# Kernel tuning notes

Measured on AMD Instinct MI355X. Metric: run time of the kernel, lower is better.

The kernel has to match this reference:

```python
import jax, jax.numpy as jnp
import numpy as np

B, N, D, H, HID = 8, 512, 512, 8, 2048


def setup_inputs() -> dict:
    key = jax.random.key(0)
    ks = jax.random.split(key, 8)
    s = 0.02
    p = lambda i, shape: jax.random.normal(ks[i], shape, jnp.float32) * s
    return dict(
        x=jax.random.normal(ks[0], (B, N, D), jnp.float32),
        Wq=p(1, (D, D)), bq=jnp.zeros((D,), jnp.float32),
        Wk=p(2, (D, D)), bk=jnp.zeros((D,), jnp.float32),
        Wv=p(3, (D, D)), bv=jnp.zeros((D,), jnp.float32),
        Wsig=p(4, (H, D)), bsig=jnp.zeros((H,), jnp.float32),
        ln1_g=jnp.ones((D,), jnp.float32), ln1_b=jnp.zeros((D,), jnp.float32),
        W1=p(5, (HID, D)), b1=jnp.zeros((HID,), jnp.float32),
        W2=p(6, (D, HID)), b2=jnp.zeros((D,), jnp.float32),
        ln2_g=jnp.ones((D,), jnp.float32), ln2_b=jnp.zeros((D,), jnp.float32),
    )


def _ln(z, g, b, eps=1e-5):
    m = jnp.mean(z, axis=-1, keepdims=True)
    v = jnp.var(z, axis=-1, keepdims=True)
    return (z - m) * jax.lax.rsqrt(v + eps) * g + b


def reference(x, Wq, bq, Wk, bk, Wv, bv, Wsig, bsig,
              ln1_g, ln1_b, W1, b1, W2, b2, ln2_g, ln2_b):
    Bb, Nn, Dd = x.shape
    Hh = bsig.shape[0]
    dh = Dd // Hh
    # --- AnomalyAttention: series attention S, Gaussian prior P, Z = S @ V ---
    Q = (x @ Wq.T + bq).reshape(Bb, Nn, Hh, dh)
    K = (x @ Wk.T + bk).reshape(Bb, Nn, Hh, dh)
    V = (x @ Wv.T + bv).reshape(Bb, Nn, Hh, dh)
    scores = jnp.einsum('bnhd,bmhd->bhnm', Q, K) / jnp.sqrt(jnp.float32(dh))
    S = jax.nn.softmax(scores, axis=-1)                       # [B,H,N,N]
    # learned positive scale sigma per (batch, position, head)
    sigma = jax.nn.softplus(x @ Wsig.T + bsig) + 1e-5         # [B,N,H]
    idx = jnp.arange(Nn, dtype=jnp.float32)
    dist2 = (idx[:, None] - idx[None, :]) ** 2                # [N,N]
    sig = jnp.transpose(sigma, (0, 2, 1))[..., None]          # [B,H,N,1]
    gauss = jnp.exp(-dist2 / (2.0 * sig * sig)) / (jnp.sqrt(2.0 * jnp.pi) * sig)
    P = gauss / jnp.sum(gauss, axis=-1, keepdims=True)        # row-normalized prior
    Zh = jnp.einsum('bhnm,bmhd->bnhd', S, V).reshape(Bb, Nn, Dd)
    # --- residual + LayerNorm + MLP(relu) + residual + LayerNorm ---
    Z = _ln(Zh + x, ln1_g, ln1_b)
    hidden = jax.nn.relu(Z @ W1.T + b1)
    x_hat = hidden @ W2.T + b2
    x_hat = _ln(x_hat + Z, ln2_g, ln2_b)
    return (x_hat, P, S)
```

## Files before the change

### kernel.cpp

```cpp
#include <hip/hip_runtime.h>
#include <cstdint>

typedef short s16x8 __attribute__((ext_vector_type(8)));
typedef float f32x4 __attribute__((ext_vector_type(4)));
using u16 = unsigned short;


__device__ __forceinline__ u16 f2bf(float f) {
    union { float f; uint32_t u; } v; v.f = f;
    uint32_t u = v.u;
    return (u16)((u + 0x7FFFu + ((u >> 16) & 1u)) >> 16);
}

__device__ __forceinline__ void gload_lds16(const void* g, void* l) {
    __builtin_amdgcn_global_load_lds(
        (const __attribute__((address_space(1))) unsigned int*)g,
        (__attribute__((address_space(3))) unsigned int*)l, 16, 0, 0);
}

__device__ __forceinline__ s16x8 pack_bf8(f32x4 a, f32x4 b) {
    union { s16x8 s; uint32_t w[4]; } o;
    uint32_t a0 = __float_as_uint(a[0]), a1 = __float_as_uint(a[1]);
    uint32_t a2 = __float_as_uint(a[2]), a3 = __float_as_uint(a[3]);
    uint32_t b0 = __float_as_uint(b[0]), b1 = __float_as_uint(b[1]);
    uint32_t b2 = __float_as_uint(b[2]), b3 = __float_as_uint(b[3]);
    o.w[0] = (a0 >> 16) | (a1 & 0xffff0000u);
    o.w[1] = (a2 >> 16) | (a3 & 0xffff0000u);
    o.w[2] = (b0 >> 16) | (b1 & 0xffff0000u);
    o.w[3] = (b2 >> 16) | (b3 & 0xffff0000u);
    return o.s;
}

__global__ __launch_bounds__(256) void k_convert_sigma(
    const float* __restrict__ x, const float* __restrict__ wq,
    const float* __restrict__ wk, const float* __restrict__ wv,
    const float* __restrict__ w1, const float* __restrict__ w2,
    const float* __restrict__ bq, const float* __restrict__ bk,
    const float* __restrict__ bv,
    const float* __restrict__ Wsig, const float* __restrict__ bsig,
    u16* __restrict__ xb, u16* __restrict__ wqb, u16* __restrict__ wkb,
    u16* __restrict__ wvb, u16* __restrict__ w1b, u16* __restrict__ w2b,
    float* __restrict__ biascat, float* __restrict__ sigT)
{
    int bk_ = blockIdx.x;
    int tid = threadIdx.x;
    if (bk_ >= 4866) {
        int row  = (int)(((bk_ - 4866) * 256 + tid) >> 6);
        int lane = tid & 63;
        const float4* xr = (const float4*)(x + (long)row * 512);
        float4 xa = xr[lane * 2], xc = xr[lane * 2 + 1];
        float xs[8] = {xa.x, xa.y, xa.z, xa.w, xc.x, xc.y, xc.z, xc.w};
        float ph[8];
#pragma unroll
        for (int h = 0; h < 8; ++h) {
            const float4* wr = (const float4*)(Wsig + h * 512);
            float4 wa = wr[lane * 2], wc = wr[lane * 2 + 1];
            ph[h] = xs[0]*wa.x + xs[1]*wa.y + xs[2]*wa.z + xs[3]*wa.w
                  + xs[4]*wc.x + xs[5]*wc.y + xs[6]*wc.z + xs[7]*wc.w;
        }
#pragma unroll
        for (int h = 0; h < 8; ++h)
#pragma unroll
            for (int m = 1; m < 64; m <<= 1)
                ph[h] += __shfl_xor(ph[h], m, 64);
        if (lane < 8) {
            float z  = ph[lane] + bsig[lane];
            float sp = fmaxf(z, 0.f) + log1pf(__expf(-fabsf(z)));
            int b = row >> 9, n = row & 511;
            sigT[(((long)b * 8 + lane) << 9) + n] = sp + 1e-5f;
        }
        return;
    }
    long g = (long)bk_ * 256 + tid;
    if (g >= 1245184) {
        long id = g - 1245184;
        if (id < 384) {
            const float* src = id < 128 ? bq : id < 256 ? bk : bv;
            ((float4*)biascat)[id] = ((const float4*)src)[id & 127];
        }
        return;
    }
    const float* src; u16* dst; long off;
    if      (g <  524288) { src = x;  dst = xb;  off = g; }
    else if (g <  589824) { src = wq; dst = wqb; off = g -  524288; }
    else if (g <  655360) { src = wk; dst = wkb; off = g -  589824; }
    else if (g <  720896) { src = wv; dst = wvb; off = g -  655360; }
    else if (g <  983040) { src = w1; dst = w1b; off = g -  720896; }
    else                  { src = w2; dst = w2b; off = g -  983040; }
    float4 v = ((const float4*)src)[off];
    ushort4 o;
    o.x = f2bf(v.x); o.y = f2bf(v.y); o.z = f2bf(v.z); o.w = f2bf(v.w);
    ((ushort4*)dst)[off] = o;
}

__global__ __launch_bounds__(256) void k_prior(
    const float* __restrict__ sigT, float* __restrict__ P)
{
    int row  = (int)((blockIdx.x * 256 + threadIdx.x) >> 6);
    int lane = threadIdx.x & 63;
    int n = row & 511;
    float s = sigT[row];
    float a = -1.0f / (2.0f * s * s);
    float e[8]; float sum = 0.f;
#pragma unroll
    for (int j = 0; j < 8; ++j) {
        float d = (float)(n - (lane * 8 + j));
        e[j] = __expf(a * d * d);
        sum += e[j];
    }
#pragma unroll
    for (int m = 1; m < 64; m <<= 1) sum += __shfl_xor(sum, m, 64);
    float r = 1.0f / sum;
    float4* dst = (float4*)(P + (long)row * 512 + lane * 8);
    dst[0] = make_float4(e[0]*r, e[1]*r, e[2]*r, e[3]*r);
    dst[1] = make_float4(e[4]*r, e[5]*r, e[6]*r, e[7]*r);
}

template<int BM, int BN, int EPI>
__global__ __launch_bounds__(256) void k_gemm_nt(
    const u16* __restrict__ A, const u16* __restrict__ B,
    const float* __restrict__ bias, void* __restrict__ C,
    int lda, int ldb, int K)
{
    constexpr int BK = 64;
    __shared__ __align__(16) u16 As[BM * BK];
    __shared__ __align__(16) u16 Bs[BN * BK];

    const u16* Ag = A + (long)blockIdx.x * BM * lda;
    const u16* Bg = B + (long)blockIdx.y * BN * ldb;

    int tid  = threadIdx.x;
    int wave = tid >> 6, lane = tid & 63;
    int wm = wave >> 1, wn = wave & 1;
    constexpr int WTM = BM / 2, WTN = BN / 2;
    constexpr int FM = WTM / 16, FN = WTN / 16;
    int r16 = lane & 15, hi8 = (lane >> 4) * 8;

    f32x4 acc[FM][FN];
#pragma unroll
    for (int i = 0; i < FM; ++i)
#pragma unroll
        for (int j = 0; j < FN; ++j) acc[i][j] = (f32x4){0.f, 0.f, 0.f, 0.f};

    constexpr int nA = BM * BK / 2048;
    constexpr int nB = BN * BK / 2048;

    for (int k0 = 0; k0 < K; k0 += BK) {
        __syncthreads();
#pragma unroll
        for (int c = 0; c < nA; ++c) {
            int e = (c * 256 + tid) * 8;
            int r = e >> 6, col = e & 63;
            gload_lds16(Ag + (long)r * lda + k0 + col, &As[e]);
        }
#pragma unroll
        for (int c = 0; c < nB; ++c) {
            int e = (c * 256 + tid) * 8;
            int r = e >> 6, col = e & 63;
            gload_lds16(Bg + (long)r * ldb + k0 + col, &Bs[e]);
        }
        __syncthreads();
#pragma unroll
        for (int kk = 0; kk < 2; ++kk) {
            s16x8 af[FM], bfr[FN];
#pragma unroll
            for (int fm = 0; fm < FM; ++fm)
                af[fm] = *(const s16x8*)&As[(wm * WTM + fm * 16 + r16) * 64 + kk * 32 + hi8];
#pragma unroll
            for (int fn = 0; fn < FN; ++fn)
                bfr[fn] = *(const s16x8*)&Bs[(wn * WTN + fn * 16 + r16) * 64 + kk * 32 + hi8];
#pragma unroll
            for (int fm = 0; fm < FM; ++fm)
#pragma unroll
                for (int fn = 0; fn < FN; ++fn)
                    acc[fm][fn] = __builtin_amdgcn_mfma_f32_16x16x32_bf16(af[fm], bfr[fn], acc[fm][fn], 0, 0, 0);
        }
    }

    int i0 = blockIdx.x * BM + wm * WTM;
    int j0 = blockIdx.y * BN + wn * WTN;
#pragma unroll
    for (int fm = 0; fm < FM; ++fm)
#pragma unroll
        for (int fn = 0; fn < FN; ++fn)
#pragma unroll
            for (int j = 0; j < 4; ++j) {
                int gi = i0 + fm * 16 + ((lane >> 4) << 2) + j;
                int gj = j0 + fn * 16 + r16;
                float v = acc[fm][fn][j];
                if constexpr (EPI == 3) {
                    v = fmaxf(v + bias[gj], 0.f);
                    ((u16*)C)[(long)gi * 2048 + gj] = f2bf(v);
                } else if constexpr (EPI == 4) {
                    ((float*)C)[(long)gi * 512 + gj] = v + bias[gj];
                } else {
                    v += bias[gj];
                    int mat = gj >> 9, cj = gj & 511;
                    int h = cj >> 6, d = cj & 63, b = gi >> 9, n = gi & 511;
                    u16* base = (u16*)C;
                    if (mat == 0)
                        base[(((long)(b * 8 + h) * 512 + n) << 6) + d] = f2bf(v);
                    else if (mat == 1)
                        (base + 2097152)[(((long)(b * 8 + h) * 512 + n) << 6) + d] = f2bf(v);
                    else
                        (base + 4194304)[(((long)(b * 8 + h) * 64 + d) << 9) + n] = f2bf(v);
                }
            }
}

__global__ __launch_bounds__(256) void k_attn_pv(
    const u16* __restrict__ Qb, const u16* __restrict__ Kb,
    const u16* __restrict__ Vt, float* __restrict__ S, float* __restrict__ Zh)
{
    __shared__ float Sb[4][16][260];
    int bh = blockIdx.y;
    int rb = blockIdx.x;
    int tid = threadIdx.x;
    int wave = tid >> 6, lane = tid & 63;
    int r16 = lane & 15, g4 = lane >> 4, hi8 = g4 * 8;

    const u16* Qg = Qb + ((long)bh * 512 + rb * 64 + wave * 16) * 64;
    const u16* Kg = Kb + (long)bh * 512 * 64;
    const u16* Vg = Vt + (long)bh * 64 * 512;

    s16x8 qa[2];
    qa[0] = *(const s16x8*)(Qg + r16 * 64 + hi8);
    qa[1] = *(const s16x8*)(Qg + r16 * 64 + 32 + hi8);

    f32x4 acc[32];
#pragma unroll
    for (int t = 0; t < 32; ++t) acc[t] = (f32x4){0.f, 0.f, 0.f, 0.f};

#pragma unroll
    for (int ch = 0; ch < 4; ++ch)
#pragma unroll
        for (int kk = 0; kk < 2; ++kk)
#pragma unroll
            for (int fn = 0; fn < 8; ++fn) {
                s16x8 b = *(const s16x8*)(Kg + (long)(ch * 128 + fn * 16 + r16) * 64 + kk * 32 + hi8);
                acc[ch * 8 + fn] = __builtin_amdgcn_mfma_f32_16x16x32_bf16(qa[kk], b, acc[ch * 8 + fn], 0, 0, 0);
            }

    float mx[4] = {-1e30f, -1e30f, -1e30f, -1e30f};
#pragma unroll
    for (int t = 0; t < 32; ++t)
#pragma unroll
        for (int j = 0; j < 4; ++j) mx[j] = fmaxf(mx[j], acc[t][j]);
#pragma unroll
    for (int j = 0; j < 4; ++j)
#pragma unroll
        for (int m = 1; m < 16; m <<= 1) mx[j] = fmaxf(mx[j], __shfl_xor(mx[j], m, 64));

    float sum[4] = {0.f, 0.f, 0.f, 0.f};
#pragma unroll
    for (int t = 0; t < 32; ++t)
#pragma unroll
        for (int j = 0; j < 4; ++j) {
            float p = __expf(0.125f * (acc[t][j] - mx[j]));
            acc[t][j] = p;
            sum[j] += p;
        }
#pragma unroll
    for (int j = 0; j < 4; ++j) {
#pragma unroll
        for (int m = 1; m < 16; m <<= 1) sum[j] += __shfl_xor(sum[j], m, 64);
        sum[j] = 1.0f / sum[j];
    }
#pragma unroll
    for (int t = 0; t < 32; ++t)
#pragma unroll
        for (int j = 0; j < 4; ++j) acc[t][j] *= sum[j];

    long sbase = ((long)bh * 512 + rb * 64 + wave * 16) * 512;
#pragma unroll
    for (int t = 0; t < 32; ++t) {
        int col = t * 16 + r16;
#pragma unroll
        for (int j = 0; j < 4; ++j)
            S[sbase + (long)(g4 * 4 + j) * 512 + col] = acc[t][j];
    }

    f32x4 zacc[4];
#pragma unroll
    for (int fn = 0; fn < 4; ++fn) zacc[fn] = (f32x4){0.f, 0.f, 0.f, 0.f};

#pragma unroll
    for (int p = 0; p < 2; ++p) {
#pragma unroll
        for (int t = 0; t < 16; ++t)
#pragma unroll
            for (int j = 0; j < 4; ++j)
                Sb[wave][g4 * 4 + j][t * 16 + r16] = acc[p * 16 + t][j];
#pragma unroll
        for (int kk = 0; kk < 8; ++kk) {
            f32x4 lo = *(const f32x4*)&Sb[wave][r16][kk * 32 + hi8];
            f32x4 hi = *(const f32x4*)&Sb[wave][r16][kk * 32 + hi8 + 4];
            s16x8 pa = pack_bf8(lo, hi);
#pragma unroll
            for (int fn = 0; fn < 4; ++fn) {
                s16x8 vb = *(const s16x8*)(Vg + (long)(fn * 16 + r16) * 512 + p * 256 + kk * 32 + hi8);
                zacc[fn] = __builtin_amdgcn_mfma_f32_16x16x32_bf16(pa, vb, zacc[fn], 0, 0, 0);
            }
        }
    }

    long zb = ((long)(bh >> 3) * 512 + rb * 64 + wave * 16) * 512 + (bh & 7) * 64;
#pragma unroll
    for (int fn = 0; fn < 4; ++fn)
#pragma unroll
        for (int j = 0; j < 4; ++j)
            Zh[zb + (long)(g4 * 4 + j) * 512 + fn * 16 + r16] = zacc[fn][j];
}

template<bool WBF>
__global__ __launch_bounds__(256) void k_ln(
    const float* __restrict__ a, const float* __restrict__ b,
    const float* __restrict__ g, const float* __restrict__ bt,
    float* __restrict__ y, u16* __restrict__ yb)
{
    int row  = (int)((blockIdx.x * 256 + threadIdx.x) >> 6);
    int lane = threadIdx.x & 63;
    const float4* ar = (const float4*)(a + (long)row * 512);
    const float4* br = (const float4*)(b + (long)row * 512);
    float4 a0 = ar[lane * 2], a1 = ar[lane * 2 + 1];
    float4 b0 = br[lane * 2], b1 = br[lane * 2 + 1];
    float v[8] = {a0.x + b0.x, a0.y + b0.y, a0.z + b0.z, a0.w + b0.w,
                  a1.x + b1.x, a1.y + b1.y, a1.z + b1.z, a1.w + b1.w};
    float s = 0.f, q = 0.f;
#pragma unroll
    for (int j = 0; j < 8; ++j) { s += v[j]; q += v[j] * v[j]; }
#pragma unroll
    for (int m = 1; m < 64; m <<= 1) {
        s += __shfl_xor(s, m, 64);
        q += __shfl_xor(q, m, 64);
    }
    float mean = s * (1.f / 512.f);
    float var  = q * (1.f / 512.f) - mean * mean;
    float rstd = rsqrtf(var + 1e-5f);
    const float4* gr = (const float4*)(g + lane * 8);
    const float4* tr = (const float4*)(bt + lane * 8);
    float4 g0 = gr[0], g1 = gr[1], t0 = tr[0], t1 = tr[1];
    float gg[8] = {g0.x, g0.y, g0.z, g0.w, g1.x, g1.y, g1.z, g1.w};
    float tt[8] = {t0.x, t0.y, t0.z, t0.w, t1.x, t1.y, t1.z, t1.w};
    float o[8];
#pragma unroll
    for (int j = 0; j < 8; ++j) o[j] = (v[j] - mean) * rstd * gg[j] + tt[j];
    float4* yr = (float4*)(y + (long)row * 512 + lane * 8);
    yr[0] = make_float4(o[0], o[1], o[2], o[3]);
    yr[1] = make_float4(o[4], o[5], o[6], o[7]);
    if constexpr (WBF) {
        s16x8 ob;
#pragma unroll
        for (int j = 0; j < 8; ++j) ob[j] = (short)f2bf(o[j]);
        *(s16x8*)(yb + (long)row * 512 + lane * 8) = ob;
    }
}

extern "C" void kernel_launch(void* const* d_in, const int* in_sizes, int n_in,
                              void* d_out, int out_size, void* d_ws, size_t ws_size,
                              hipStream_t stream)
{
    const float* x    = (const float*)d_in[0];
    const float* Wq   = (const float*)d_in[1];
    const float* bq   = (const float*)d_in[2];
    const float* Wk   = (const float*)d_in[3];
    const float* bk   = (const float*)d_in[4];
    const float* Wv   = (const float*)d_in[5];
    const float* bv   = (const float*)d_in[6];
    const float* Wsig = (const float*)d_in[7];
    const float* bsig = (const float*)d_in[8];
    const float* g1   = (const float*)d_in[9];
    const float* be1  = (const float*)d_in[10];
    const float* W1   = (const float*)d_in[11];
    const float* b1   = (const float*)d_in[12];
    const float* W2   = (const float*)d_in[13];
    const float* b2   = (const float*)d_in[14];
    const float* g2   = (const float*)d_in[15];
    const float* be2  = (const float*)d_in[16];

    float* out_xhat = (float*)d_out;
    float* out_P    = out_xhat + 2097152;
    float* out_S    = out_P + 16777216;

    char* ws = (char*)d_ws;
    u16*   xb   = (u16*)(ws + 0);
    u16*   Qb   = (u16*)(ws + 4194304);
    u16*   hid  = (u16*)(ws + 0);
    u16*   Wqb  = (u16*)(ws + 16777216);
    u16*   W1b  = (u16*)(ws + 18350080);
    u16*   W2b  = (u16*)(ws + 20447232);
    float* sigT = (float*)(ws + 22544384);
    float* Zh   = (float*)(ws + 22675456);
    float* bcat = (float*)(ws + 22675456);
    float* x2   = (float*)(ws + 22675456);
    float* Z    = (float*)(ws + 31064064);
    u16*   Zb   = (u16*)(ws + 39452672);

    u16* Wkb = Wqb + 262144;
    u16* Wvb = Wqb + 524288;

    k_convert_sigma<<<5890, 256, 0, stream>>>(x, Wq, Wk, Wv, W1, W2, bq, bk, bv,
                                              Wsig, bsig,
                                              xb, Wqb, Wkb, Wvb, W1b, W2b,
                                              bcat, sigT);
    k_prior<<<8192, 256, 0, stream>>>(sigT, out_P);

    k_gemm_nt<128,128,5><<<dim3(32,12,1),256,0,stream>>>(
        xb, Wqb, bcat, Qb, 512, 512, 512);

    k_attn_pv<<<dim3(8,64),256,0,stream>>>(Qb, Qb + 2097152, Qb + 4194304, out_S, Zh);

    k_ln<true><<<1024,256,0,stream>>>(Zh, x, g1, be1, Z, Zb);

    k_gemm_nt<128,128,3><<<dim3(32,16,1),256,0,stream>>>(Zb, W1b, b1, hid, 512, 512, 512);

    k_gemm_nt<64,64,4><<<dim3(64,8,1),256,0,stream>>>(hid, W2b, b2, x2, 2048, 2048, 2048);

    k_ln<false><<<1024,256,0,stream>>>(x2, Z, g2, be2, out_xhat, nullptr);
}
```

Before: 155.5 us.

## Double-buffer GEMM with swizzled LDS, 512 threads, fuse prior into attention

The GEMM kernel now uses 8 waves and double-buffered LDS tiles. The next K tile is loaded while the current one is consumed, and an XOR swizzle on the LDS layout avoids bank conflicts. The separate Gaussian prior kernel is removed and its computation is appended to the attention kernel, which saves one launch. The W2 GEMM tile shape changes to 64x128. Register and LDS pressure rise, and the attention kernel gets longer.

```diff
diff --git a/kernel.cpp b/kernel.cpp
--- a/kernel.cpp
+++ b/kernel.cpp
@@ -93,48 +93,25 @@
     ((ushort4*)dst)[off] = o;
 }
 
-__global__ __launch_bounds__(256) void k_prior(
-    const float* __restrict__ sigT, float* __restrict__ P)
-{
-    int row  = (int)((blockIdx.x * 256 + threadIdx.x) >> 6);
-    int lane = threadIdx.x & 63;
-    int n = row & 511;
-    float s = sigT[row];
-    float a = -1.0f / (2.0f * s * s);
-    float e[8]; float sum = 0.f;
-#pragma unroll
-    for (int j = 0; j < 8; ++j) {
-        float d = (float)(n - (lane * 8 + j));
-        e[j] = __expf(a * d * d);
-        sum += e[j];
-    }
-#pragma unroll
-    for (int m = 1; m < 64; m <<= 1) sum += __shfl_xor(sum, m, 64);
-    float r = 1.0f / sum;
-    float4* dst = (float4*)(P + (long)row * 512 + lane * 8);
-    dst[0] = make_float4(e[0]*r, e[1]*r, e[2]*r, e[3]*r);
-    dst[1] = make_float4(e[4]*r, e[5]*r, e[6]*r, e[7]*r);
-}
-
 template<int BM, int BN, int EPI>
-__global__ __launch_bounds__(256) void k_gemm_nt(
+__global__ __launch_bounds__(512) void k_gemm_nt(
     const u16* __restrict__ A, const u16* __restrict__ B,
     const float* __restrict__ bias, void* __restrict__ C,
     int lda, int ldb, int K)
 {
     constexpr int BK = 64;
-    __shared__ __align__(16) u16 As[BM * BK];
-    __shared__ __align__(16) u16 Bs[BN * BK];
+    __shared__ __align__(16) u16 As[2][BM * BK];
+    __shared__ __align__(16) u16 Bs[2][BN * BK];
 
     const u16* Ag = A + (long)blockIdx.x * BM * lda;
     const u16* Bg = B + (long)blockIdx.y * BN * ldb;
 
     int tid  = threadIdx.x;
     int wave = tid >> 6, lane = tid & 63;
-    int wm = wave >> 1, wn = wave & 1;
-    constexpr int WTM = BM / 2, WTN = BN / 2;
+    int wm = wave >> 2, wn = wave & 3;
+    constexpr int WTM = BM / 2, WTN = BN / 4;
     constexpr int FM = WTM / 16, FN = WTN / 16;
-    int r16 = lane & 15, hi8 = (lane >> 4) * 8;
+    int r16 = lane & 15, g4 = lane >> 4;
 
     f32x4 acc[FM][FN];
 #pragma unroll
@@ -142,39 +119,55 @@
 #pragma unroll
         for (int j = 0; j < FN; ++j) acc[i][j] = (f32x4){0.f, 0.f, 0.f, 0.f};
 
-    constexpr int nA = BM * BK / 2048;
-    constexpr int nB = BN * BK / 2048;
-
-    for (int k0 = 0; k0 < K; k0 += BK) {
-        __syncthreads();
+    constexpr int nA = BM * BK / (512 * 8);
+    constexpr int nB = BN * BK / (512 * 8);
+
+    auto stage = [&](int buf, int k0) {
 #pragma unroll
         for (int c = 0; c < nA; ++c) {
-            int e = (c * 256 + tid) * 8;
-            int r = e >> 6, col = e & 63;
-            gload_lds16(Ag + (long)r * lda + k0 + col, &As[e]);
+            int e = c * 512 + tid;
+            int r = e >> 3, s = e & 7;
+            gload_lds16(Ag + (long)r * lda + k0 + ((s ^ (r & 7)) * 8),
+                        &As[buf][e * 8]);
         }
 #pragma unroll
         for (int c = 0; c < nB; ++c) {
-            int e = (c * 256 + tid) * 8;
-            int r = e >> 6, col = e & 63;
-            gload_lds16(Bg + (long)r * ldb + k0 + col, &Bs[e]);
-        }
-        __syncthreads();
+            int e = c * 512 + tid;
+            int r = e >> 3, s = e & 7;
+            gload_lds16(Bg + (long)r * ldb + k0 + ((s ^ (r & 7)) * 8),
+                        &Bs[buf][e * 8]);
+        }
+    };
+
+    stage(0, 0);
+    __syncthreads();
+    int cur = 0;
+    const int NT = K / BK;
+    for (int t = 0; t < NT; ++t) {
+        if (t + 1 < NT) stage(cur ^ 1, (t + 1) * BK);
 #pragma unroll
         for (int kk = 0; kk < 2; ++kk) {
             s16x8 af[FM], bfr[FN];
 #pragma unroll
-            for (int fm = 0; fm < FM; ++fm)
-                af[fm] = *(const s16x8*)&As[(wm * WTM + fm * 16 + r16) * 64 + kk * 32 + hi8];
-#pragma unroll
-            for (int fn = 0; fn < FN; ++fn)
-                bfr[fn] = *(const s16x8*)&Bs[(wn * WTN + fn * 16 + r16) * 64 + kk * 32 + hi8];
+            for (int fm = 0; fm < FM; ++fm) {
+                int row = wm * WTM + fm * 16 + r16;
+                int slot = (kk * 4 + g4) ^ (row & 7);
+                af[fm] = *(const s16x8*)&As[cur][row * 64 + slot * 8];
+            }
+#pragma unroll
+            for (int fn = 0; fn < FN; ++fn) {
+                int row = wn * WTN + fn * 16 + r16;
+                int slot = (kk * 4 + g4) ^ (row & 7);
+                bfr[fn] = *(const s16x8*)&Bs[cur][row * 64 + slot * 8];
+            }
 #pragma unroll
             for (int fm = 0; fm < FM; ++fm)
 #pragma unroll
                 for (int fn = 0; fn < FN; ++fn)
                     acc[fm][fn] = __builtin_amdgcn_mfma_f32_16x16x32_bf16(af[fm], bfr[fn], acc[fm][fn], 0, 0, 0);
         }
+        __syncthreads();
+        cur ^= 1;
     }
 
     int i0 = blockIdx.x * BM + wm * WTM;
@@ -185,7 +178,7 @@
         for (int fn = 0; fn < FN; ++fn)
 #pragma unroll
             for (int j = 0; j < 4; ++j) {
-                int gi = i0 + fm * 16 + ((lane >> 4) << 2) + j;
+                int gi = i0 + fm * 16 + (g4 << 2) + j;
                 int gj = j0 + fn * 16 + r16;
                 float v = acc[fm][fn][j];
                 if constexpr (EPI == 3) {
@@ -210,7 +203,8 @@
 
 __global__ __launch_bounds__(256) void k_attn_pv(
     const u16* __restrict__ Qb, const u16* __restrict__ Kb,
-    const u16* __restrict__ Vt, float* __restrict__ S, float* __restrict__ Zh)
+    const u16* __restrict__ Vt, const float* __restrict__ sigT,
+    float* __restrict__ S, float* __restrict__ Zh, float* __restrict__ P)
 {
     __shared__ float Sb[4][16][260];
     int bh = blockIdx.y;
@@ -310,6 +304,28 @@
 #pragma unroll
         for (int j = 0; j < 4; ++j)
             Zh[zb + (long)(g4 * 4 + j) * 512 + fn * 16 + r16] = zacc[fn][j];
+
+    const float* sig = sigT + (long)bh * 512 + rb * 64 + wave * 16;
+    long pbase = ((long)bh * 512 + rb * 64 + wave * 16) * 512;
+#pragma unroll
+    for (int rr = 0; rr < 16; ++rr) {
+        float s = sig[rr];
+        float a = -1.0f / (2.0f * s * s);
+        int n = rb * 64 + wave * 16 + rr;
+        float e[8]; float sum2 = 0.f;
+#pragma unroll
+        for (int j = 0; j < 8; ++j) {
+            float d = (float)(n - (lane * 8 + j));
+            e[j] = __expf(a * d * d);
+            sum2 += e[j];
+        }
+#pragma unroll
+        for (int m = 1; m < 64; m <<= 1) sum2 += __shfl_xor(sum2, m, 64);
+        float r = 1.0f / sum2;
+        float4* dst = (float4*)(P + pbase + (long)rr * 512 + lane * 8);
+        dst[0] = make_float4(e[0]*r, e[1]*r, e[2]*r, e[3]*r);
+        dst[1] = make_float4(e[4]*r, e[5]*r, e[6]*r, e[7]*r);
+    }
 }
 
 template<bool WBF>
@@ -403,18 +419,18 @@
                                               Wsig, bsig,
                                               xb, Wqb, Wkb, Wvb, W1b, W2b,
                                               bcat, sigT);
-    k_prior<<<8192, 256, 0, stream>>>(sigT, out_P);
-
-    k_gemm_nt<128,128,5><<<dim3(32,12,1),256,0,stream>>>(
+
+    k_gemm_nt<128,128,5><<<dim3(32,12,1),512,0,stream>>>(
         xb, Wqb, bcat, Qb, 512, 512, 512);
 
-    k_attn_pv<<<dim3(8,64),256,0,stream>>>(Qb, Qb + 2097152, Qb + 4194304, out_S, Zh);
+    k_attn_pv<<<dim3(8,64),256,0,stream>>>(Qb, Qb + 2097152, Qb + 4194304,
+                                           sigT, out_S, Zh, out_P);
 
     k_ln<true><<<1024,256,0,stream>>>(Zh, x, g1, be1, Z, Zb);
 
-    k_gemm_nt<128,128,3><<<dim3(32,16,1),256,0,stream>>>(Zb, W1b, b1, hid, 512, 512, 512);
-
-    k_gemm_nt<64,64,4><<<dim3(64,8,1),256,0,stream>>>(hid, W2b, b2, x2, 2048, 2048, 2048);
+    k_gemm_nt<128,128,3><<<dim3(32,16,1),512,0,stream>>>(Zb, W1b, b1, hid, 512, 512, 512);
+
+    k_gemm_nt<64,128,4><<<dim3(64,4,1),512,0,stream>>>(hid, W2b, b2, x2, 2048, 2048, 2048);
 
     k_ln<false><<<1024,256,0,stream>>>(x2, Z, g2, be2, out_xhat, nullptr);
 }
```

Measured after the change: 140.9 us. 1.1x faster.
